# Optimization experiments

Hardware: AMD Instinct MI355X
Metric: run time of the kernel (lower is better)

The kernel has to match this reference:

```python
import jax, jax.numpy as jnp
import numpy as np


def setup_inputs() -> dict:
    key = jax.random.key(0)
    k1, k2 = jax.random.split(key)
    flow = jax.random.normal(k1, (4, 2, 256, 256), dtype=jnp.float32)   # [B,2,H,W] per-pixel flow over dt
    spike = jax.random.uniform(k2, (4, 64, 256, 256), dtype=jnp.float32)  # [B,C,H,W] spike voxel grid
    return {"flow": flow, "spike": spike}


def _splat(vals, xn, yn, H, W):
    """Forward bilinear splat of vals [H,W] to continuous coords (xn,yn) [H,W]."""
    x0 = jnp.floor(xn)
    y0 = jnp.floor(yn)
    wx = xn - x0  # fractional weights (differentiable w.r.t. flow)
    wy = yn - y0
    x0i = x0.astype(jnp.int32)
    y0i = y0.astype(jnp.int32)
    out = jnp.zeros(H * W, dtype=vals.dtype)
    corners = (
        (0, 0, (1.0 - wx) * (1.0 - wy)),
        (1, 0, wx * (1.0 - wy)),
        (0, 1, (1.0 - wx) * wy),
        (1, 1, wx * wy),
    )
    for dx, dy, w in corners:
        xi = x0i + dx
        yi = y0i + dy
        valid = (xi >= 0) & (xi < W) & (yi >= 0) & (yi < H)
        idx = jnp.clip(yi, 0, H - 1) * W + jnp.clip(xi, 0, W - 1)
        out = out.at[idx.ravel()].add(jnp.where(valid, w * vals, 0.0).ravel())
    return out.reshape(H, W)


def spike_warp_mid(spike, flow, dt):
    """Warp each time bin c by flow * (c - mid)/dt toward the middle timestamp (bilinear splat)."""
    B, C, H, W = spike.shape
    mid = (C - 1) / 2.0
    yy, xx = jnp.meshgrid(jnp.arange(H, dtype=spike.dtype),
                          jnp.arange(W, dtype=spike.dtype), indexing='ij')
    s = (jnp.arange(C, dtype=spike.dtype) - mid) / jnp.asarray(dt, spike.dtype)  # [C]
    u = flow[:, 0][:, None]  # [B,1,H,W]
    v = flow[:, 1][:, None]
    xn = xx + u * s[None, :, None, None]  # [B,C,H,W]
    yn = yy + v * s[None, :, None, None]
    splat_bc = jax.vmap(jax.vmap(lambda va, xa, ya: _splat(va, xa, ya, H, W)))
    return splat_bc(spike, xn, yn)  # [B,C,H,W]


def reference(flow, spike):
    B, C, H, W = spike.shape
    spike_warped = spike_warp_mid(spike, flow, dt=64)
    # Faithful to original: sum over BATCH dim inside per-batch loop (same each iter),
    # so loss = (B * -var) / B = -var(spike_image) with unbiased variance.
    spike_image = jnp.sum(spike_warped, axis=0)  # [C,H,W]
    loss = -jnp.var(spike_image - jnp.mean(spike_image), ddof=1)
    return loss
```

## Files before the change

kernel.cpp:

```cpp
#include <hip/hip_runtime.h>

constexpr int B = 4, C = 64, H = 256, W = 256;
constexpr int HW = H * W;
constexpr long long N_TOT = (long long)C * HW;

constexpr int TS = 16;
constexpr int R = 4;
constexpr int SW = TS + 2 * R;
constexpr int SAREA = SW * SW;
constexpr int NBLK = 256 * 8;

__global__ __launch_bounds__(256) void fused_kernel(
    const float* __restrict__ flow,
    const float* __restrict__ spike,
    double* __restrict__ partials) {
  __shared__ float2 uv[SAREA];
  __shared__ float4 spkA[SAREA];
  __shared__ float4 spkB[SAREA];
  __shared__ float wmax[4];
  __shared__ double red[8];

  const int bid = blockIdx.x;
  const int tile = bid & 255;
  const int j = bid >> 8;
  const int tx0 = (tile & 15) * TS;
  const int ty0 = (tile >> 4) * TS;
  const int tid = threadIdx.x;
  const int qx = tid & 15, qy = tid >> 4;

  float smag[4];
  int cn[4], cp[4];
#pragma unroll
  for (int t = 0; t < 4; ++t) {
    int k = 4 * j + t;
    smag[t] = ((float)k + 0.5f) * (1.0f / 64.0f);
    cn[t] = 31 - k;
    cp[t] = 32 + k;
  }

  float acc[8];
#pragma unroll
  for (int t = 0; t < 8; ++t) acc[t] = 0.f;

  const int qpos = (qy + R) * SW + (qx + R);

  for (int b = 0; b < B; ++b) {
    const float* fu = flow + (size_t)b * 2 * HW;
    const float* fv = fu + HW;
    const float* spb = spike + (size_t)b * C * HW;

    float m = 0.f;
    for (int pos = tid; pos < SAREA; pos += 256) {
      int py = pos / SW;
      int px = pos - py * SW;
      int gy = ty0 + py - R;
      int gx = tx0 + px - R;
      float u = 0.f, v = 0.f;
      float4 a = {0.f, 0.f, 0.f, 0.f};
      float4 d = {0.f, 0.f, 0.f, 0.f};
      if ((unsigned)gy < (unsigned)H && (unsigned)gx < (unsigned)W) {
        int gp = gy * W + gx;
        u = fu[gp];
        v = fv[gp];
        a.x = spb[(size_t)cn[0] * HW + gp];
        a.y = spb[(size_t)cn[1] * HW + gp];
        a.z = spb[(size_t)cn[2] * HW + gp];
        a.w = spb[(size_t)cn[3] * HW + gp];
        d.x = spb[(size_t)cp[0] * HW + gp];
        d.y = spb[(size_t)cp[1] * HW + gp];
        d.z = spb[(size_t)cp[2] * HW + gp];
        d.w = spb[(size_t)cp[3] * HW + gp];
      }
      uv[pos] = make_float2(u, v);
      spkA[pos] = a;
      spkB[pos] = d;
      m = fmaxf(m, fmaxf(fabsf(u), fabsf(v)));
    }
    for (int off = 32; off > 0; off >>= 1)
      m = fmaxf(m, __shfl_down(m, off, 64));
    if ((tid & 63) == 0) wmax[tid >> 6] = m;
    __syncthreads();
    float mb = fmaxf(fmaxf(wmax[0], wmax[1]), fmaxf(wmax[2], wmax[3]));
    int r = min((int)(1.0f + mb * smag[3]), R);

    for (int dy = -r; dy <= r; ++dy) {
      float fdy = (float)dy;
      for (int dx = -r; dx <= r; ++dx) {
        int pp = qpos + dy * SW + dx;
        float2 u2 = uv[pp];
        float4 va = spkA[pp];
        float4 vb = spkB[pp];
        float fdx = (float)dx;
        const float* vaf = &va.x;
        const float* vbf = &vb.x;
#pragma unroll
        for (int t = 0; t < 4; ++t) {
          float sm = smag[t];
          float txn = fmaxf(0.f, 1.f - fabsf(fmaf(u2.x, -sm, fdx)));
          float tyn = fmaxf(0.f, 1.f - fabsf(fmaf(u2.y, -sm, fdy)));
          acc[t] = fmaf(txn * tyn, vaf[t], acc[t]);
          float txp = fmaxf(0.f, 1.f - fabsf(fmaf(u2.x, sm, fdx)));
          float typ = fmaxf(0.f, 1.f - fabsf(fmaf(u2.y, sm, fdy)));
          acc[4 + t] = fmaf(txp * typ, vbf[t], acc[4 + t]);
        }
      }
    }
    __syncthreads();
  }

  double ls = 0.0, lq = 0.0;
#pragma unroll
  for (int t = 0; t < 8; ++t) {
    double a = (double)acc[t];
    ls += a;
    lq += a * a;
  }
  for (int off = 32; off > 0; off >>= 1) {
    ls += __shfl_down(ls, off, 64);
    lq += __shfl_down(lq, off, 64);
  }
  int wave = tid >> 6;
  if ((tid & 63) == 0) { red[wave * 2] = ls; red[wave * 2 + 1] = lq; }
  __syncthreads();
  if (tid == 0) {
    partials[2 * bid] = red[0] + red[2] + red[4] + red[6];
    partials[2 * bid + 1] = red[1] + red[3] + red[5] + red[7];
  }
}

__global__ __launch_bounds__(256) void finalize_kernel(
    const double* __restrict__ partials, float* __restrict__ out) {
  double s = 0.0, q = 0.0;
  for (int i = threadIdx.x; i < NBLK; i += 256) {
    s += partials[2 * i];
    q += partials[2 * i + 1];
  }
  for (int off = 32; off > 0; off >>= 1) {
    s += __shfl_down(s, off, 64);
    q += __shfl_down(q, off, 64);
  }
  __shared__ double ss[4], qq[4];
  int lane = threadIdx.x & 63;
  int wave = threadIdx.x >> 6;
  if (lane == 0) { ss[wave] = s; qq[wave] = q; }
  __syncthreads();
  if (threadIdx.x == 0) {
    double sum = ss[0] + ss[1] + ss[2] + ss[3];
    double sq = qq[0] + qq[1] + qq[2] + qq[3];
    double n = (double)N_TOT;
    double var = (sq - sum * sum / n) / (n - 1.0);
    out[0] = (float)(-var);
  }
}

extern "C" void kernel_launch(void* const* d_in, const int* in_sizes, int n_in,
                              void* d_out, int out_size, void* d_ws, size_t ws_size,
                              hipStream_t stream) {
  const float* flow = (const float*)d_in[0];
  const float* spike = (const float*)d_in[1];
  float* out = (float*)d_out;
  double* partials = (double*)d_ws;

  fused_kernel<<<dim3(NBLK), dim3(256), 0, stream>>>(flow, spike, partials);
  finalize_kernel<<<1, dim3(256), 0, stream>>>(partials, out);
}
```

Before: 161.1 us.

## Prefetch next batch into registers, pad LDS rows, use per-wave separate x/y radii

Loads for the next batch are now issued into registers before the gather loop of the current batch, so global latency overlaps with compute. The LDS tile rows are padded to stride 25 to reduce bank conflicts. The single block-wide flow max is replaced by per-row u/v maxima gathered with LDS atomics. Each wave then derives separate, tighter x and y search radii from only the rows it touches, which shrinks the gather window. The cost is more registers for the prefetch buffers and extra atomics and row-max bookkeeping.

```diff
diff --git a/kernel.cpp b/kernel.cpp
--- a/kernel.cpp
+++ b/kernel.cpp
@@ -6,7 +6,8 @@
 
 constexpr int TS = 16;
 constexpr int R = 4;
-constexpr int SW = TS + 2 * R;
+constexpr int SW = 24;
+constexpr int PS = 25;
 constexpr int SAREA = SW * SW;
 constexpr int NBLK = 256 * 8;
 
@@ -14,10 +15,10 @@
     const float* __restrict__ flow,
     const float* __restrict__ spike,
     double* __restrict__ partials) {
-  __shared__ float2 uv[SAREA];
-  __shared__ float4 spkA[SAREA];
-  __shared__ float4 spkB[SAREA];
-  __shared__ float wmax[4];
+  __shared__ float2 uv[SW * PS];
+  __shared__ float4 spkA[SW * PS];
+  __shared__ float4 spkB[SW * PS];
+  __shared__ int2 rowmax[2][SW];
   __shared__ double red[8];
 
   const int bid = blockIdx.x;
@@ -27,66 +28,109 @@
   const int ty0 = (tile >> 4) * TS;
   const int tid = threadIdx.x;
   const int qx = tid & 15, qy = tid >> 4;
+  const int wave = tid >> 6;
 
   float smag[4];
-  int cn[4], cp[4];
-#pragma unroll
-  for (int t = 0; t < 4; ++t) {
-    int k = 4 * j + t;
-    smag[t] = ((float)k + 0.5f) * (1.0f / 64.0f);
-    cn[t] = 31 - k;
-    cp[t] = 32 + k;
-  }
+#pragma unroll
+  for (int t = 0; t < 4; ++t)
+    smag[t] = ((float)(4 * j + t) + 0.5f) * (1.0f / 64.0f);
+  const int cn0 = 31 - 4 * j;
+  const int cp0 = 32 + 4 * j;
 
   float acc[8];
 #pragma unroll
   for (int t = 0; t < 8; ++t) acc[t] = 0.f;
 
-  const int qpos = (qy + R) * SW + (qx + R);
-
-  for (int b = 0; b < B; ++b) {
+  bool c_act[3], c_val[3];
+  int c_apos[3], c_row[3], c_gp[3];
+#pragma unroll
+  for (int k = 0; k < 3; ++k) {
+    int pos = tid + 256 * k;
+    c_act[k] = pos < SAREA;
+    int row = pos / SW;
+    int col = pos - row * SW;
+    c_apos[k] = row * PS + col;
+    c_row[k] = row;
+    int gy = ty0 + row - R, gx = tx0 + col - R;
+    c_val[k] = c_act[k] & ((unsigned)gy < (unsigned)H) & ((unsigned)gx < (unsigned)W);
+    c_gp[k] = gy * W + gx;
+  }
+
+  float p_u[3], p_v[3];
+  float4 p_a[3], p_b[3];
+
+  auto prefetch = [&](int b) {
     const float* fu = flow + (size_t)b * 2 * HW;
     const float* fv = fu + HW;
     const float* spb = spike + (size_t)b * C * HW;
-
-    float m = 0.f;
-    for (int pos = tid; pos < SAREA; pos += 256) {
-      int py = pos / SW;
-      int px = pos - py * SW;
-      int gy = ty0 + py - R;
-      int gx = tx0 + px - R;
+#pragma unroll
+    for (int k = 0; k < 3; ++k) {
       float u = 0.f, v = 0.f;
       float4 a = {0.f, 0.f, 0.f, 0.f};
       float4 d = {0.f, 0.f, 0.f, 0.f};
-      if ((unsigned)gy < (unsigned)H && (unsigned)gx < (unsigned)W) {
-        int gp = gy * W + gx;
+      if (c_val[k]) {
+        int gp = c_gp[k];
         u = fu[gp];
         v = fv[gp];
-        a.x = spb[(size_t)cn[0] * HW + gp];
-        a.y = spb[(size_t)cn[1] * HW + gp];
-        a.z = spb[(size_t)cn[2] * HW + gp];
-        a.w = spb[(size_t)cn[3] * HW + gp];
-        d.x = spb[(size_t)cp[0] * HW + gp];
-        d.y = spb[(size_t)cp[1] * HW + gp];
-        d.z = spb[(size_t)cp[2] * HW + gp];
-        d.w = spb[(size_t)cp[3] * HW + gp];
+        a.x = spb[(size_t)cn0 * HW + gp];
+        a.y = spb[(size_t)(cn0 - 1) * HW + gp];
+        a.z = spb[(size_t)(cn0 - 2) * HW + gp];
+        a.w = spb[(size_t)(cn0 - 3) * HW + gp];
+        d.x = spb[(size_t)cp0 * HW + gp];
+        d.y = spb[(size_t)(cp0 + 1) * HW + gp];
+        d.z = spb[(size_t)(cp0 + 2) * HW + gp];
+        d.w = spb[(size_t)(cp0 + 3) * HW + gp];
       }
-      uv[pos] = make_float2(u, v);
-      spkA[pos] = a;
-      spkB[pos] = d;
-      m = fmaxf(m, fmaxf(fabsf(u), fabsf(v)));
-    }
-    for (int off = 32; off > 0; off >>= 1)
-      m = fmaxf(m, __shfl_down(m, off, 64));
-    if ((tid & 63) == 0) wmax[tid >> 6] = m;
+      p_u[k] = u; p_v[k] = v; p_a[k] = a; p_b[k] = d;
+    }
+  };
+
+  auto store_lds = [&](int b) {
+    int bs = b & 1;
+#pragma unroll
+    for (int k = 0; k < 3; ++k) {
+      if (c_act[k]) {
+        int ap = c_apos[k];
+        uv[ap] = make_float2(p_u[k], p_v[k]);
+        spkA[ap] = p_a[k];
+        spkB[ap] = p_b[k];
+        atomicMax(&rowmax[bs][c_row[k]].x, __float_as_int(fabsf(p_u[k])));
+        atomicMax(&rowmax[bs][c_row[k]].y, __float_as_int(fabsf(p_v[k])));
+      }
+    }
+  };
+
+  if (tid < SW) {
+    rowmax[0][tid] = make_int2(0, 0);
+    rowmax[1][tid] = make_int2(0, 0);
+  }
+  prefetch(0);
+  __syncthreads();
+
+  const int qpos = (qy + R) * PS + (qx + R);
+  const int wr0 = 4 * wave;
+
+  for (int b = 0; b < B; ++b) {
+    store_lds(b);
     __syncthreads();
-    float mb = fmaxf(fmaxf(wmax[0], wmax[1]), fmaxf(wmax[2], wmax[3]));
-    int r = min((int)(1.0f + mb * smag[3]), R);
-
-    for (int dy = -r; dy <= r; ++dy) {
+
+    int mu = 0, mv = 0;
+#pragma unroll
+    for (int i = 0; i < 12; ++i) {
+      int2 rmv = rowmax[b & 1][wr0 + i];
+      mu = max(mu, rmv.x);
+      mv = max(mv, rmv.y);
+    }
+    float fmu = __int_as_float(mu), fmv = __int_as_float(mv);
+    int rx = min((int)(1.0f + fmu * smag[3]), R);
+    int ry = min((int)(1.0f + fmv * smag[3]), R);
+
+    if (b + 1 < B) prefetch(b + 1);
+
+    for (int dy = -ry; dy <= ry; ++dy) {
       float fdy = (float)dy;
-      for (int dx = -r; dx <= r; ++dx) {
-        int pp = qpos + dy * SW + dx;
+      for (int dx = -rx; dx <= rx; ++dx) {
+        int pp = qpos + dy * PS + dx;
         float2 u2 = uv[pp];
         float4 va = spkA[pp];
         float4 vb = spkB[pp];
@@ -105,6 +149,8 @@
         }
       }
     }
+
+    if (tid < SW) rowmax[(b + 1) & 1][tid] = make_int2(0, 0);
     __syncthreads();
   }
 
@@ -119,7 +165,6 @@
     ls += __shfl_down(ls, off, 64);
     lq += __shfl_down(lq, off, 64);
   }
-  int wave = tid >> 6;
   if ((tid & 63) == 0) { red[wave * 2] = ls; red[wave * 2 + 1] = lq; }
   __syncthreads();
   if (tid == 0) {
```

New measurement: 164.7 us. +2.3%, slower.
